# Kernel optimization log

Hardware: AMD Instinct MI355X
Metric: run time of the kernel (lower is better)

## Reference

```python
import jax, jax.numpy as jnp
import numpy as np

ALPHA = 1.0

def setup_inputs() -> dict:
    key = jax.random.key(0)
    k1, k2 = jax.random.split(key)
    x = jax.random.normal(k1, (65536, 512), dtype=jnp.float32)
    clusters = jax.random.normal(k2, (256, 512), dtype=jnp.float32)
    return {"x": x, "clusters": clusters}

def reference(x, clusters):
    # Squared Euclidean distance to each centroid via the GEMM expansion
    x2 = jnp.sum(x * x, axis=1, keepdims=True)            # (B, 1)
    c2 = jnp.sum(clusters * clusters, axis=1)             # (K,)
    cross = x @ clusters.T                                # (B, K) GEMM
    d2 = jnp.maximum(x2 + c2 - 2.0 * cross, 0.0)          # (B, K)
    # Student-t kernel (DEC soft assignment)
    q = 1.0 / (1.0 + d2 / ALPHA)
    q = q ** ((ALPHA + 1.0) / 2.0)
    q = q / jnp.sum(q, axis=1, keepdims=True)             # row-normalize
    return q
```

## Files before the change

kernel.cpp:

```cpp
#include <hip/hip_runtime.h>


typedef __attribute__((ext_vector_type(4))) short short4v;
typedef __attribute__((ext_vector_type(8))) short short8v;
typedef __attribute__((ext_vector_type(4))) float f32x4;

#define DDIM 512
#define KCL  256
#define BM   64
#define BK   32
#define NT   512
#define NTILES 16
#define BTILE  (KCL*BK)

__device__ __forceinline__ short f2bf(float f) {
    union { float f; unsigned u; } v; v.f = f;
    unsigned r = v.u + 0x7FFFu + ((v.u >> 16) & 1u);
    return (short)(r >> 16);
}

__device__ __forceinline__ void glds16(const void* g, void* l) {
    __builtin_amdgcn_global_load_lds(
        (const __attribute__((address_space(1))) unsigned int*)g,
        (__attribute__((address_space(3))) unsigned int*)l, 16, 0, 0);
}

__global__ void conv_clusters(const float* __restrict__ cl, short* __restrict__ wsB) {
    const int u = blockIdx.x * blockDim.x + threadIdx.x;
    const int img = u >> 10, gi = u & 1023;
    const int g = gi >> 6, lq = (gi >> 4) & 3, l15 = gi & 15;
    const float* src = cl + (size_t)(g * 16 + l15) * DDIM + img * 32 + lq * 8;
    float4 a = *(const float4*)src;
    float4 b = *(const float4*)(src + 4);
    short8v s;
    s[0]=f2bf(a.x); s[1]=f2bf(a.y); s[2]=f2bf(a.z); s[3]=f2bf(a.w);
    s[4]=f2bf(b.x); s[5]=f2bf(b.y); s[6]=f2bf(b.z); s[7]=f2bf(b.w);
    *(short8v*)&wsB[(size_t)u * 8] = s;
}

__global__ void calc_c2(const float* __restrict__ cl, float* __restrict__ c2) {
    const int b = blockIdx.x, l = threadIdx.x;
    const float* src = cl + (size_t)b * DDIM + l * 8;
    float4 a = *(const float4*)src, c = *(const float4*)(src + 4);
    float s = a.x*a.x+a.y*a.y+a.z*a.z+a.w*a.w + c.x*c.x+c.y*c.y+c.z*c.z+c.w*c.w;
    s += __shfl_xor(s,1); s += __shfl_xor(s,2); s += __shfl_xor(s,4);
    s += __shfl_xor(s,8); s += __shfl_xor(s,16); s += __shfl_xor(s,32);
    if (l == 0) c2[b] = s;
}

__global__ __launch_bounds__(NT, 4)
void dec_main(const float* __restrict__ x, const short* __restrict__ wsB,
              const float* __restrict__ wsC2, float* __restrict__ out) {
    __shared__ __align__(16) short lA[2][BM * BK];
    __shared__ __align__(16) short lB[2][BTILE];
    __shared__ float s_x2[BM];
    __shared__ float s_c2[KCL];
    __shared__ float s_rs[4][BM];

    const int t    = threadIdx.x;
    const int lane = t & 63;
    const int w    = t >> 6;
    const int rg   = w >> 2;
    const int cg   = w & 3;
    const int l15  = lane & 15, lq = lane >> 4;
    const int row0 = blockIdx.x * BM;

    const int srow = t >> 3, sk4 = (t & 7) << 2;
    const float* xbase = x + (size_t)(row0 + srow) * DDIM + sk4;
    const int aidx = (((srow >> 4) * 4 + (sk4 >> 3)) * 16 + (srow & 15)) * 8 + (sk4 & 4);

    if (t < KCL) s_c2[t] = wsC2[t];

    float x2p = 0.f;
    f32x4 acc[2][4];
#pragma unroll
    for (int m = 0; m < 2; ++m)
#pragma unroll
        for (int n = 0; n < 4; ++n) acc[m][n] = (f32x4){0.f, 0.f, 0.f, 0.f};

    auto writeA = [&](short* dst, float4 v) {
        x2p += v.x*v.x + v.y*v.y + v.z*v.z + v.w*v.w;
        short4v s;
        s[0]=f2bf(v.x); s[1]=f2bf(v.y); s[2]=f2bf(v.z); s[3]=f2bf(v.w);
        *(short4v*)&dst[aidx] = s;
    };
    auto gldsB = [&](short* dst, int tile) {
        const short* src = wsB + (size_t)tile * BTILE;
        glds16(src + t * 8, dst + t * 8);
        glds16(src + 4096 + t * 8, dst + 4096 + t * 8);
    };
    auto mstep = [&](const short* A, const short* Bt) {
        const short* Ab = A + rg * 1024;
        const short* Bb = Bt + cg * 2048;
        short8v a0 = *(const short8v*)&Ab[lane * 8];
        short8v a1 = *(const short8v*)&Ab[512 + lane * 8];
        short8v b0 = *(const short8v*)&Bb[lane * 8];
        short8v b1 = *(const short8v*)&Bb[512  + lane * 8];
        short8v b2 = *(const short8v*)&Bb[1024 + lane * 8];
        short8v b3 = *(const short8v*)&Bb[1536 + lane * 8];
        acc[0][0] = __builtin_amdgcn_mfma_f32_16x16x32_bf16(a0, b0, acc[0][0], 0,0,0);
        acc[0][1] = __builtin_amdgcn_mfma_f32_16x16x32_bf16(a0, b1, acc[0][1], 0,0,0);
        acc[0][2] = __builtin_amdgcn_mfma_f32_16x16x32_bf16(a0, b2, acc[0][2], 0,0,0);
        acc[0][3] = __builtin_amdgcn_mfma_f32_16x16x32_bf16(a0, b3, acc[0][3], 0,0,0);
        acc[1][0] = __builtin_amdgcn_mfma_f32_16x16x32_bf16(a1, b0, acc[1][0], 0,0,0);
        acc[1][1] = __builtin_amdgcn_mfma_f32_16x16x32_bf16(a1, b1, acc[1][1], 0,0,0);
        acc[1][2] = __builtin_amdgcn_mfma_f32_16x16x32_bf16(a1, b2, acc[1][2], 0,0,0);
        acc[1][3] = __builtin_amdgcn_mfma_f32_16x16x32_bf16(a1, b3, acc[1][3], 0,0,0);
    };

    float4 xrA = *(const float4*)(xbase);
    gldsB(lB[0], 0);
    float4 xrB = *(const float4*)(xbase + BK);
    writeA(lA[0], xrA);

    for (int tt = 0; tt < NTILES; tt += 2) {
        __syncthreads();
        writeA(lA[1], xrB);
        gldsB(lB[1], tt + 1);
        if (tt < NTILES - 2) xrA = *(const float4*)(xbase + (tt + 2) * BK);
        mstep(lA[0], lB[0]);
        __syncthreads();
        if (tt < NTILES - 2) { writeA(lA[0], xrA); gldsB(lB[0], tt + 2); }
        if (tt + 3 < NTILES) xrB = *(const float4*)(xbase + (tt + 3) * BK);
        mstep(lA[1], lB[1]);
    }

    x2p += __shfl_xor(x2p, 1); x2p += __shfl_xor(x2p, 2); x2p += __shfl_xor(x2p, 4);
    if ((t & 7) == 0) s_x2[srow] = x2p;
    __syncthreads();

#pragma unroll
    for (int m = 0; m < 2; ++m)
#pragma unroll
        for (int n = 0; n < 4; ++n) {
            const float c2v = s_c2[cg * 64 + n * 16 + l15];
#pragma unroll
            for (int r = 0; r < 4; ++r) {
                const int rw = rg * 32 + m * 16 + lq * 4 + r;
                float d2 = fmaxf(s_x2[rw] + c2v - 2.0f * acc[m][n][r], 0.0f);
                acc[m][n][r] = 1.0f / (1.0f + d2);
            }
        }

#pragma unroll
    for (int m = 0; m < 2; ++m)
#pragma unroll
        for (int r = 0; r < 4; ++r) {
            float p = acc[m][0][r] + acc[m][1][r] + acc[m][2][r] + acc[m][3][r];
            p += __shfl_xor(p, 1); p += __shfl_xor(p, 2);
            p += __shfl_xor(p, 4); p += __shfl_xor(p, 8);
            if (l15 == 0) s_rs[cg][rg * 32 + m * 16 + lq * 4 + r] = p;
        }
    __syncthreads();

#pragma unroll
    for (int m = 0; m < 2; ++m)
#pragma unroll
        for (int r = 0; r < 4; ++r) {
            const int rw = rg * 32 + m * 16 + lq * 4 + r;
            const float rinv = 1.0f / (s_rs[0][rw] + s_rs[1][rw] + s_rs[2][rw] + s_rs[3][rw]);
            float* o = out + (size_t)(row0 + rw) * KCL + cg * 64 + l15;
#pragma unroll
            for (int n = 0; n < 4; ++n)
                o[n * 16] = acc[m][n][r] * rinv;
        }
}

extern "C" void kernel_launch(void* const* d_in, const int* in_sizes, int n_in,
                              void* d_out, int out_size, void* d_ws, size_t ws_size,
                              hipStream_t stream) {
    const float* x  = (const float*)d_in[0];
    const float* cl = (const float*)d_in[1];
    float* out = (float*)d_out;
    short* wsB  = (short*)d_ws;
    float* wsC2 = (float*)((char*)d_ws + (size_t)NTILES * BTILE * sizeof(short));

    conv_clusters<<<64, 256, 0, stream>>>(cl, wsB);
    calc_c2<<<KCL, 64, 0, stream>>>(cl, wsC2);
    const int B = in_sizes[0] / DDIM;
    dec_main<<<B / BM, NT, 0, stream>>>(x, wsB, wsC2, out);
}
```

Baseline: 55.66 us.

## Make each wave load its own A tile and B fragments directly, removing block barriers

The main loop no longer shares LDS tiles across the block. Each wave now loads its own x rows, converts them to bf16 into a private swizzled 4-deep LDS ring, and reads its B fragments from global memory straight into registers with double buffering, so there are no __syncthreads in the K loop. The two prep kernels are merged into one launch, and c2 is read from global memory in the epilogue. In exchange, each x row is loaded and converted by all four column-group waves instead of once, register pressure rises, and B traffic goes through L2 per wave rather than being shared through LDS.

```diff
diff --git a/kernel.cpp b/kernel.cpp
--- a/kernel.cpp
+++ b/kernel.cpp
@@ -1,4 +1,5 @@
 #include <hip/hip_runtime.h>
+#include <hip/hip_bf16.h>
 
 
 typedef __attribute__((ext_vector_type(4))) short short4v;
@@ -8,139 +9,152 @@
 #define DDIM 512
 #define KCL  256
 #define BM   64
-#define BK   32
 #define NT   512
 #define NTILES 16
-#define BTILE  (KCL*BK)
+#define BTILE  8192
 
 __device__ __forceinline__ short f2bf(float f) {
-    union { float f; unsigned u; } v; v.f = f;
-    unsigned r = v.u + 0x7FFFu + ((v.u >> 16) & 1u);
-    return (short)(r >> 16);
+    __hip_bfloat16 h = __float2bfloat16(f);
+    return __builtin_bit_cast(short, h);
 }
 
-__device__ __forceinline__ void glds16(const void* g, void* l) {
-    __builtin_amdgcn_global_load_lds(
-        (const __attribute__((address_space(1))) unsigned int*)g,
-        (__attribute__((address_space(3))) unsigned int*)l, 16, 0, 0);
-}
-
-__global__ void conv_clusters(const float* __restrict__ cl, short* __restrict__ wsB) {
-    const int u = blockIdx.x * blockDim.x + threadIdx.x;
-    const int img = u >> 10, gi = u & 1023;
-    const int g = gi >> 6, lq = (gi >> 4) & 3, l15 = gi & 15;
-    const float* src = cl + (size_t)(g * 16 + l15) * DDIM + img * 32 + lq * 8;
-    float4 a = *(const float4*)src;
-    float4 b = *(const float4*)(src + 4);
-    short8v s;
-    s[0]=f2bf(a.x); s[1]=f2bf(a.y); s[2]=f2bf(a.z); s[3]=f2bf(a.w);
-    s[4]=f2bf(b.x); s[5]=f2bf(b.y); s[6]=f2bf(b.z); s[7]=f2bf(b.w);
-    *(short8v*)&wsB[(size_t)u * 8] = s;
-}
-
-__global__ void calc_c2(const float* __restrict__ cl, float* __restrict__ c2) {
-    const int b = blockIdx.x, l = threadIdx.x;
-    const float* src = cl + (size_t)b * DDIM + l * 8;
-    float4 a = *(const float4*)src, c = *(const float4*)(src + 4);
-    float s = a.x*a.x+a.y*a.y+a.z*a.z+a.w*a.w + c.x*c.x+c.y*c.y+c.z*c.z+c.w*c.w;
-    s += __shfl_xor(s,1); s += __shfl_xor(s,2); s += __shfl_xor(s,4);
-    s += __shfl_xor(s,8); s += __shfl_xor(s,16); s += __shfl_xor(s,32);
-    if (l == 0) c2[b] = s;
+__global__ void prep(const float* __restrict__ cl, short* __restrict__ wsB,
+                     float* __restrict__ wsC2) {
+    const int t = threadIdx.x;
+    if (blockIdx.x < 64) {
+        const int u = blockIdx.x * 256 + t;
+        const int img = u >> 10, gi = u & 1023;
+        const int g = gi >> 6, lq = (gi >> 4) & 3, l15 = gi & 15;
+        const float* src = cl + (size_t)(g * 16 + l15) * DDIM + img * 32 + lq * 8;
+        float4 a = *(const float4*)src;
+        float4 b = *(const float4*)(src + 4);
+        short8v s;
+        s[0]=f2bf(a.x); s[1]=f2bf(a.y); s[2]=f2bf(a.z); s[3]=f2bf(a.w);
+        s[4]=f2bf(b.x); s[5]=f2bf(b.y); s[6]=f2bf(b.z); s[7]=f2bf(b.w);
+        *(short8v*)&wsB[(size_t)u * 8] = s;
+    } else {
+        const int cidx = (blockIdx.x - 64) * 16 + (t >> 4);
+        const int j = t & 15;
+        const float* src = cl + (size_t)cidx * DDIM + j * 32;
+        float s = 0.f;
+#pragma unroll
+        for (int i = 0; i < 8; ++i) {
+            float4 v = ((const float4*)src)[i];
+            s += v.x*v.x + v.y*v.y + v.z*v.z + v.w*v.w;
+        }
+        s += __shfl_xor(s, 1); s += __shfl_xor(s, 2);
+        s += __shfl_xor(s, 4); s += __shfl_xor(s, 8);
+        if (j == 0) wsC2[cidx] = s;
+    }
 }
 
 __global__ __launch_bounds__(NT, 4)
 void dec_main(const float* __restrict__ x, const short* __restrict__ wsB,
               const float* __restrict__ wsC2, float* __restrict__ out) {
-    __shared__ __align__(16) short lA[2][BM * BK];
-    __shared__ __align__(16) short lB[2][BTILE];
+    __shared__ __align__(16) short lA[8][4][1024];
     __shared__ float s_x2[BM];
-    __shared__ float s_c2[KCL];
     __shared__ float s_rs[4][BM];
 
-    const int t    = threadIdx.x;
-    const int lane = t & 63;
-    const int w    = t >> 6;
-    const int rg   = w >> 2;
-    const int cg   = w & 3;
-    const int l15  = lane & 15, lq = lane >> 4;
+    const int t = threadIdx.x, lane = t & 63, w = t >> 6;
+    const int rg = w >> 2, cg = w & 3;
+    const int l15 = lane & 15, lq = lane >> 4;
+    const int rsub = lane >> 2, q4 = lane & 3;
     const int row0 = blockIdx.x * BM;
 
-    const int srow = t >> 3, sk4 = (t & 7) << 2;
-    const float* xbase = x + (size_t)(row0 + srow) * DDIM + sk4;
-    const int aidx = (((srow >> 4) * 4 + (sk4 >> 3)) * 16 + (srow & 15)) * 8 + (sk4 & 4);
+    const float* xb0 = x + (size_t)(row0 + rg*32 + rsub) * DDIM + q4*4;
+    const float* xb1 = xb0 + (size_t)16 * DDIM;
+    const short* bb = wsB + (size_t)(cg*4) * 512 + (size_t)lane * 8;
+    short* const myA = &lA[w][0][0];
+    const int cs  = (rsub & 3) << 3;
+    const int fs0 = (lq * 8) ^ ((l15 & 3) << 3);
 
-    if (t < KCL) s_c2[t] = wsC2[t];
-
-    float x2p = 0.f;
     f32x4 acc[2][4];
 #pragma unroll
     for (int m = 0; m < 2; ++m)
 #pragma unroll
-        for (int n = 0; n < 4; ++n) acc[m][n] = (f32x4){0.f, 0.f, 0.f, 0.f};
+        for (int n = 0; n < 4; ++n) acc[m][n] = (f32x4){0.f,0.f,0.f,0.f};
+    float x2a = 0.f, x2b = 0.f;
 
-    auto writeA = [&](short* dst, float4 v) {
-        x2p += v.x*v.x + v.y*v.y + v.z*v.z + v.w*v.w;
-        short4v s;
-        s[0]=f2bf(v.x); s[1]=f2bf(v.y); s[2]=f2bf(v.z); s[3]=f2bf(v.w);
-        *(short4v*)&dst[aidx] = s;
-    };
-    auto gldsB = [&](short* dst, int tile) {
-        const short* src = wsB + (size_t)tile * BTILE;
-        glds16(src + t * 8, dst + t * 8);
-        glds16(src + 4096 + t * 8, dst + 4096 + t * 8);
-    };
-    auto mstep = [&](const short* A, const short* Bt) {
-        const short* Ab = A + rg * 1024;
-        const short* Bb = Bt + cg * 2048;
-        short8v a0 = *(const short8v*)&Ab[lane * 8];
-        short8v a1 = *(const short8v*)&Ab[512 + lane * 8];
-        short8v b0 = *(const short8v*)&Bb[lane * 8];
-        short8v b1 = *(const short8v*)&Bb[512  + lane * 8];
-        short8v b2 = *(const short8v*)&Bb[1024 + lane * 8];
-        short8v b3 = *(const short8v*)&Bb[1536 + lane * 8];
-        acc[0][0] = __builtin_amdgcn_mfma_f32_16x16x32_bf16(a0, b0, acc[0][0], 0,0,0);
-        acc[0][1] = __builtin_amdgcn_mfma_f32_16x16x32_bf16(a0, b1, acc[0][1], 0,0,0);
-        acc[0][2] = __builtin_amdgcn_mfma_f32_16x16x32_bf16(a0, b2, acc[0][2], 0,0,0);
-        acc[0][3] = __builtin_amdgcn_mfma_f32_16x16x32_bf16(a0, b3, acc[0][3], 0,0,0);
-        acc[1][0] = __builtin_amdgcn_mfma_f32_16x16x32_bf16(a1, b0, acc[1][0], 0,0,0);
-        acc[1][1] = __builtin_amdgcn_mfma_f32_16x16x32_bf16(a1, b1, acc[1][1], 0,0,0);
-        acc[1][2] = __builtin_amdgcn_mfma_f32_16x16x32_bf16(a1, b2, acc[1][2], 0,0,0);
-        acc[1][3] = __builtin_amdgcn_mfma_f32_16x16x32_bf16(a1, b3, acc[1][3], 0,0,0);
-    };
+    short8v B[2][4];
+    float4 xv[2][4];
 
-    float4 xrA = *(const float4*)(xbase);
-    gldsB(lB[0], 0);
-    float4 xrB = *(const float4*)(xbase + BK);
-    writeA(lA[0], xrA);
+#define LOADB(tt, slot)                                                          \
+    {  _Pragma("unroll")                                                         \
+       for (int n = 0; n < 4; ++n)                                              \
+           B[slot][n] = *(const short8v*)(bb + (size_t)(tt) * BTILE + n * 512); }
 
-    for (int tt = 0; tt < NTILES; tt += 2) {
-        __syncthreads();
-        writeA(lA[1], xrB);
-        gldsB(lB[1], tt + 1);
-        if (tt < NTILES - 2) xrA = *(const float4*)(xbase + (tt + 2) * BK);
-        mstep(lA[0], lB[0]);
-        __syncthreads();
-        if (tt < NTILES - 2) { writeA(lA[0], xrA); gldsB(lB[0], tt + 2); }
-        if (tt + 3 < NTILES) xrB = *(const float4*)(xbase + (tt + 3) * BK);
-        mstep(lA[1], lB[1]);
+#define LOADX(tt, slot)                                                          \
+    {  xv[slot][0] = *(const float4*)(xb0 + (tt) * 32);                          \
+       xv[slot][1] = *(const float4*)(xb0 + (tt) * 32 + 16);                     \
+       xv[slot][2] = *(const float4*)(xb1 + (tt) * 32);                          \
+       xv[slot][3] = *(const float4*)(xb1 + (tt) * 32 + 16); }
+
+#define CVTW(buf, slot)                                                          \
+    {  short* dst = myA + (buf) * 1024;                                          \
+       float4 a = xv[slot][0], b2 = xv[slot][1], c = xv[slot][2], d = xv[slot][3];\
+       short4v sa, sb, sc, sd;                                                   \
+       sa[0]=f2bf(a.x); sa[1]=f2bf(a.y); sa[2]=f2bf(a.z); sa[3]=f2bf(a.w);       \
+       sb[0]=f2bf(b2.x); sb[1]=f2bf(b2.y); sb[2]=f2bf(b2.z); sb[3]=f2bf(b2.w);   \
+       sc[0]=f2bf(c.x); sc[1]=f2bf(c.y); sc[2]=f2bf(c.z); sc[3]=f2bf(c.w);       \
+       sd[0]=f2bf(d.x); sd[1]=f2bf(d.y); sd[2]=f2bf(d.z); sd[3]=f2bf(d.w);       \
+       *(short4v*)&dst[rsub*32        + ((q4*4)      ^ cs)] = sa;                \
+       *(short4v*)&dst[rsub*32        + ((16 + q4*4) ^ cs)] = sb;                \
+       *(short4v*)&dst[(16+rsub)*32   + ((q4*4)      ^ cs)] = sc;                \
+       *(short4v*)&dst[(16+rsub)*32   + ((16 + q4*4) ^ cs)] = sd;                \
+       x2a += a.x*a.x + a.y*a.y + a.z*a.z + a.w*a.w                              \
+            + b2.x*b2.x + b2.y*b2.y + b2.z*b2.z + b2.w*b2.w;                     \
+       x2b += c.x*c.x + c.y*c.y + c.z*c.z + c.w*c.w                              \
+            + d.x*d.x + d.y*d.y + d.z*d.z + d.w*d.w; }
+
+    LOADB(0, 0);
+    LOADX(0, 0); LOADX(1, 1);
+    LOADB(1, 1);
+    CVTW(0, 0); CVTW(1, 1);
+    LOADX(2, 0); LOADX(3, 1);
+
+#pragma unroll
+    for (int tt = 0; tt < NTILES; ++tt) {
+        const short* buf = myA + (tt & 3) * 1024;
+        short8v a0 = *(const short8v*)&buf[(l15)      * 32 + fs0];
+        short8v a1 = *(const short8v*)&buf[(16 + l15) * 32 + fs0];
+        const int sl = tt & 1;
+        acc[0][0] = __builtin_amdgcn_mfma_f32_16x16x32_bf16(a0, B[sl][0], acc[0][0], 0,0,0);
+        acc[0][1] = __builtin_amdgcn_mfma_f32_16x16x32_bf16(a0, B[sl][1], acc[0][1], 0,0,0);
+        acc[0][2] = __builtin_amdgcn_mfma_f32_16x16x32_bf16(a0, B[sl][2], acc[0][2], 0,0,0);
+        acc[0][3] = __builtin_amdgcn_mfma_f32_16x16x32_bf16(a0, B[sl][3], acc[0][3], 0,0,0);
+        acc[1][0] = __builtin_amdgcn_mfma_f32_16x16x32_bf16(a1, B[sl][0], acc[1][0], 0,0,0);
+        acc[1][1] = __builtin_amdgcn_mfma_f32_16x16x32_bf16(a1, B[sl][1], acc[1][1], 0,0,0);
+        acc[1][2] = __builtin_amdgcn_mfma_f32_16x16x32_bf16(a1, B[sl][2], acc[1][2], 0,0,0);
+        acc[1][3] = __builtin_amdgcn_mfma_f32_16x16x32_bf16(a1, B[sl][3], acc[1][3], 0,0,0);
+        if (tt + 2 < NTILES) {
+            LOADB(tt + 2, sl);
+            CVTW((tt + 2) & 3, sl);
+        }
+        if (tt + 4 < NTILES) LOADX(tt + 4, sl);
     }
 
-    x2p += __shfl_xor(x2p, 1); x2p += __shfl_xor(x2p, 2); x2p += __shfl_xor(x2p, 4);
-    if ((t & 7) == 0) s_x2[srow] = x2p;
+    x2a += __shfl_xor(x2a, 1); x2a += __shfl_xor(x2a, 2);
+    x2b += __shfl_xor(x2b, 1); x2b += __shfl_xor(x2b, 2);
+    if (cg == 0 && q4 == 0) {
+        s_x2[rg*32 + rsub]      = x2a;
+        s_x2[rg*32 + 16 + rsub] = x2b;
+    }
     __syncthreads();
+
+    float c2a[4];
+#pragma unroll
+    for (int n = 0; n < 4; ++n) c2a[n] = wsC2[cg*64 + n*16 + l15];
 
 #pragma unroll
     for (int m = 0; m < 2; ++m)
 #pragma unroll
-        for (int n = 0; n < 4; ++n) {
-            const float c2v = s_c2[cg * 64 + n * 16 + l15];
+        for (int n = 0; n < 4; ++n)
 #pragma unroll
             for (int r = 0; r < 4; ++r) {
-                const int rw = rg * 32 + m * 16 + lq * 4 + r;
-                float d2 = fmaxf(s_x2[rw] + c2v - 2.0f * acc[m][n][r], 0.0f);
+                const int rw = rg*32 + m*16 + lq*4 + r;
+                float d2 = fmaxf(s_x2[rw] + c2a[n] - 2.0f * acc[m][n][r], 0.0f);
                 acc[m][n][r] = 1.0f / (1.0f + d2);
             }
-        }
 
 #pragma unroll
     for (int m = 0; m < 2; ++m)
@@ -149,7 +163,7 @@
             float p = acc[m][0][r] + acc[m][1][r] + acc[m][2][r] + acc[m][3][r];
             p += __shfl_xor(p, 1); p += __shfl_xor(p, 2);
             p += __shfl_xor(p, 4); p += __shfl_xor(p, 8);
-            if (l15 == 0) s_rs[cg][rg * 32 + m * 16 + lq * 4 + r] = p;
+            if (l15 == 0) s_rs[cg][rg*32 + m*16 + lq*4 + r] = p;
         }
     __syncthreads();
 
@@ -157,9 +171,9 @@
     for (int m = 0; m < 2; ++m)
 #pragma unroll
         for (int r = 0; r < 4; ++r) {
-            const int rw = rg * 32 + m * 16 + lq * 4 + r;
+            const int rw = rg*32 + m*16 + lq*4 + r;
             const float rinv = 1.0f / (s_rs[0][rw] + s_rs[1][rw] + s_rs[2][rw] + s_rs[3][rw]);
-            float* o = out + (size_t)(row0 + rw) * KCL + cg * 64 + l15;
+            float* o = out + (size_t)(row0 + rw) * KCL + cg*64 + l15;
 #pragma unroll
             for (int n = 0; n < 4; ++n)
                 o[n * 16] = acc[m][n][r] * rinv;
@@ -175,8 +189,7 @@
     short* wsB  = (short*)d_ws;
     float* wsC2 = (float*)((char*)d_ws + (size_t)NTILES * BTILE * sizeof(short));
 
-    conv_clusters<<<64, 256, 0, stream>>>(cl, wsB);
-    calc_c2<<<KCL, 64, 0, stream>>>(cl, wsC2);
+    prep<<<80, 256, 0, stream>>>(cl, wsB, wsC2);
     const int B = in_sizes[0] / DDIM;
     dec_main<<<B / BM, NT, 0, stream>>>(x, wsB, wsC2, out);
 }
```

Measured after the change: 136.5 us. +145.2%, slower.
